# Optimization experiments

Measured on AMD Instinct MI355X. Metric: run time of the kernel, lower is better.

## Reference

```python
import jax, jax.numpy as jnp
import numpy as np

N_NODES = 50000
N_EDGES = 800000
IN_CH = 128
HEADS = 4
OUT_CH = 32
NEG_SLOPE = 0.2


def setup_inputs() -> dict:
    key = jax.random.key(0)
    ks = jax.random.split(key, 7)
    x = jax.random.normal(ks[0], (N_NODES, IN_CH), dtype=jnp.float32)
    src = jax.random.randint(ks[1], (N_EDGES,), 0, N_NODES, dtype=jnp.int32)
    dst = jax.random.randint(ks[2], (N_EDGES,), 0, N_NODES, dtype=jnp.int32)
    W = jax.random.normal(ks[3], (IN_CH, HEADS * OUT_CH), dtype=jnp.float32) * (1.0 / np.sqrt(IN_CH))
    attn_l = jax.random.normal(ks[4], (HEADS, OUT_CH), dtype=jnp.float32) * 0.1
    attn_r = jax.random.normal(ks[5], (HEADS, OUT_CH), dtype=jnp.float32) * 0.1
    bias = jnp.zeros((HEADS * OUT_CH,), dtype=jnp.float32)
    return {"x": x, "src": src, "dst": dst, "W": W, "attn_l": attn_l, "attn_r": attn_r, "bias": bias}


def reference(x, src, dst, W, attn_l, attn_r, bias):
    n = x.shape[0]
    # Linear projection -> per-head features [N, H, D]
    feat = (x @ W).reshape(n, HEADS, OUT_CH)
    # Node-level attention terms [N, H]
    el = jnp.einsum('nhd,hd->nh', feat, attn_l)
    er = jnp.einsum('nhd,hd->nh', feat, attn_r)
    # Edge attention logits [E, H]
    e = jax.nn.leaky_relu(el[src] + er[dst], negative_slope=NEG_SLOPE)
    # Segment softmax over incoming edges of each dst node
    m = jax.ops.segment_max(e, dst, num_segments=n)          # [N, H]
    m = jnp.where(jnp.isfinite(m), m, 0.0)
    ex = jnp.exp(e - m[dst])                                  # [E, H]
    s = jax.ops.segment_sum(ex, dst, num_segments=n)          # [N, H]
    alpha = ex / s[dst]                                       # [E, H]
    # Weighted message aggregation: scatter-add to dst [N, H, D]
    msg = feat[src] * alpha[:, :, None]
    out = jax.ops.segment_sum(msg, dst, num_segments=n)
    out = out + bias.reshape(HEADS, OUT_CH)
    # agg='mean' over heads -> [N, D]
    return out.mean(axis=1)
```

## Files before the change

### kernel.cpp

```cpp
#include <hip/hip_runtime.h>

#define IN_CH 128
#define NEG_SLOPE 0.2f
#define MAXDEG 64

typedef short bf16x8 __attribute__((ext_vector_type(8)));
typedef float floatx4 __attribute__((ext_vector_type(4)));

static __device__ __forceinline__ unsigned short f2bf(float f) {
    union { float f; unsigned int u; } a; a.f = f;
    unsigned int u = a.u;
    u += 0x7fffu + ((u >> 16) & 1u);
    return (unsigned short)(u >> 16);
}

__global__ void k_prep(const float* __restrict__ W, unsigned short* __restrict__ Wtb,
                       int* __restrict__ cnt, int N) {
    int i = blockIdx.x * 256 + threadIdx.x;
    if (i < N) cnt[(size_t)i << 4] = 0;
    if (i < 128 * 128) {
        int n = i >> 7, k = i & 127;
        Wtb[i] = f2bf(W[(size_t)k * 128 + n]);
    }
}

__global__ __launch_bounds__(256) void k_fused(const float* __restrict__ x,
                                               const unsigned short* __restrict__ Wtb,
                                               const float* __restrict__ attn_l,
                                               const float* __restrict__ attn_r,
                                               unsigned short* __restrict__ featb,
                                               float* __restrict__ el,
                                               float* __restrict__ er, int N,
                                               const int* __restrict__ src,
                                               const int* __restrict__ dst,
                                               int* __restrict__ cnt,
                                               unsigned short* __restrict__ esrc_pad, int E,
                                               int GB, int RB) {
    __shared__ __align__(16) unsigned short Al[16 * 136];
    __shared__ float elpart[2][8][16];
    int b = blockIdx.x;
    int M2 = 2 * (GB < RB ? GB : RB);
    bool is_edge;
    int part;
    if (b < M2) { is_edge = (b & 1); part = b >> 1; }
    else        { is_edge = (RB > GB); part = (M2 >> 1) + (b - M2); }
    if (is_edge) {
        int e = part * 256 + threadIdx.x;
        if (e < E) {
            int dn = dst[e];
            int sv = src[e];
            int r = atomicAdd(&cnt[(size_t)dn << 4], 1);
            if (r < MAXDEG) esrc_pad[(size_t)dn * MAXDEG + r] = (unsigned short)sv;
        }
        return;
    }
    int m0 = part * 16;
    const float4* xt = (const float4*)(x + (size_t)m0 * 128);
#pragma unroll
    for (int i = 0; i < 2; ++i) {
        int f4i = threadIdx.x + 256 * i;
        float4 u = xt[f4i];
        int f = f4i * 4;
        int row = f >> 7, col = f & 127;
        ushort4 pk;
        pk.x = f2bf(u.x); pk.y = f2bf(u.y); pk.z = f2bf(u.z); pk.w = f2bf(u.w);
        *(ushort4*)(Al + row * 136 + col) = pk;
    }
    __syncthreads();
    int wave = threadIdx.x >> 6;
    int lane = threadIdx.x & 63;
    int l15 = lane & 15;
    int quad = lane >> 4;
    int n0 = wave * 16;
    int n1 = wave * 16 + 64;
    const unsigned short* ap = Al + l15 * 136 + quad * 8;
    const unsigned short* bp0 = Wtb + (size_t)(n0 + l15) * 128 + quad * 8;
    const unsigned short* bp1 = Wtb + (size_t)(n1 + l15) * 128 + quad * 8;
    floatx4 acc0 = {0.f, 0.f, 0.f, 0.f};
    floatx4 acc1 = {0.f, 0.f, 0.f, 0.f};
#pragma unroll
    for (int kk = 0; kk < 4; ++kk) {
        bf16x8 a  = *(const bf16x8*)(ap + kk * 32);
        bf16x8 b0 = *(const bf16x8*)(bp0 + kk * 32);
        bf16x8 b1 = *(const bf16x8*)(bp1 + kk * 32);
        acc0 = __builtin_amdgcn_mfma_f32_16x16x32_bf16(a, b0, acc0, 0, 0, 0);
        acc1 = __builtin_amdgcn_mfma_f32_16x16x32_bf16(a, b1, acc1, 0, 0, 0);
    }
    float al0 = attn_l[n0 + l15], al1 = attn_l[n1 + l15];
    float ar0 = attn_r[n0 + l15], ar1 = attn_r[n1 + l15];
    float pl0[4], pl1[4], pr0[4], pr1[4];
#pragma unroll
    for (int r = 0; r < 4; ++r) {
        pl0[r] = acc0[r] * al0; pl1[r] = acc1[r] * al1;
        pr0[r] = acc0[r] * ar0; pr1[r] = acc1[r] * ar1;
#pragma unroll
        for (int m = 1; m <= 8; m <<= 1) {
            pl0[r] += __shfl_xor(pl0[r], m);
            pl1[r] += __shfl_xor(pl1[r], m);
            pr0[r] += __shfl_xor(pr0[r], m);
            pr1[r] += __shfl_xor(pr1[r], m);
        }
    }
    if (l15 == 0) {
#pragma unroll
        for (int r = 0; r < 4; ++r) {
            int row = quad * 4 + r;
            elpart[0][wave][row]     = pl0[r];
            elpart[0][wave + 4][row] = pl1[r];
            elpart[1][wave][row]     = pr0[r];
            elpart[1][wave + 4][row] = pr1[r];
        }
    }
#pragma unroll
    for (int r = 0; r < 4; ++r) {
        size_t row = (size_t)(m0 + quad * 4 + r) * 128;
        featb[row + n0 + l15] = f2bf(acc0[r]);
        featb[row + n1 + l15] = f2bf(acc1[r]);
    }
    __syncthreads();
    if (threadIdx.x < 128) {
        int lr = threadIdx.x >> 6;
        int t = threadIdx.x & 63;
        int row = t & 15, h = t >> 4;
        float v = elpart[lr][2 * h][row] + elpart[lr][2 * h + 1][row];
        float* dp = lr ? er : el;
        dp[(size_t)(m0 + row) * 4 + h] = v;
    }
}

__global__ __launch_bounds__(256) void k_node(const int* __restrict__ cnt,
                                              const unsigned short* __restrict__ esrc_pad,
                                              const float* __restrict__ el,
                                              const float* __restrict__ er,
                                              const unsigned short* __restrict__ featb,
                                              const float* __restrict__ bias,
                                              float* __restrict__ out, int N) {
    int n = blockIdx.x * 4 + (threadIdx.x >> 6);
    if (n >= N) return;
    int lane = threadIdx.x & 63;
    int g = lane >> 4;
    int r = lane & 15;
    int h = r >> 2;
    int deg = cnt[(size_t)n << 4];
    if (deg > MAXDEG) deg = MAXDEG;
    const unsigned short* ep = esrc_pad + (size_t)n * MAXDEG;
    float erh = er[(size_t)n * 4 + h];
    float s = 0.f;
    float a0 = 0.f, a1 = 0.f, a2 = 0.f, a3 = 0.f;
    float a4 = 0.f, a5 = 0.f, a6 = 0.f, a7 = 0.f;
    int j = g;
    int sn_c = (j < deg) ? (int)ep[j] : 0;
    float el_c = el[(size_t)sn_c * 4 + h];
    uint4 q_c = *(const uint4*)(featb + (size_t)sn_c * 128 + r * 8);
#pragma unroll 2
    for (; j < deg; j += 4) {
        int jn = j + 4;
        int sn_n = (jn < deg) ? (int)ep[jn] : 0;
        float el_n = el[(size_t)sn_n * 4 + h];
        uint4 q_n = *(const uint4*)(featb + (size_t)sn_n * 128 + r * 8);
        float t = el_c + erh;
        float e = __expf(t > 0.f ? t : NEG_SLOPE * t);
        s += e;
        a0 += e * __uint_as_float(q_c.x << 16);
        a1 += e * __uint_as_float(q_c.x & 0xffff0000u);
        a2 += e * __uint_as_float(q_c.y << 16);
        a3 += e * __uint_as_float(q_c.y & 0xffff0000u);
        a4 += e * __uint_as_float(q_c.z << 16);
        a5 += e * __uint_as_float(q_c.z & 0xffff0000u);
        a6 += e * __uint_as_float(q_c.w << 16);
        a7 += e * __uint_as_float(q_c.w & 0xffff0000u);
        sn_c = sn_n; el_c = el_n; q_c = q_n;
    }
    s  += __shfl_xor(s, 16);  s  += __shfl_xor(s, 32);
    a0 += __shfl_xor(a0, 16); a0 += __shfl_xor(a0, 32);
    a1 += __shfl_xor(a1, 16); a1 += __shfl_xor(a1, 32);
    a2 += __shfl_xor(a2, 16); a2 += __shfl_xor(a2, 32);
    a3 += __shfl_xor(a3, 16); a3 += __shfl_xor(a3, 32);
    a4 += __shfl_xor(a4, 16); a4 += __shfl_xor(a4, 32);
    a5 += __shfl_xor(a5, 16); a5 += __shfl_xor(a5, 32);
    a6 += __shfl_xor(a6, 16); a6 += __shfl_xor(a6, 32);
    a7 += __shfl_xor(a7, 16); a7 += __shfl_xor(a7, 32);
    float inv = (deg > 0) ? 0.25f / s : 0.f;
    a0 *= inv; a1 *= inv; a2 *= inv; a3 *= inv;
    a4 *= inv; a5 *= inv; a6 *= inv; a7 *= inv;
    a0 += __shfl_xor(a0, 4); a0 += __shfl_xor(a0, 8);
    a1 += __shfl_xor(a1, 4); a1 += __shfl_xor(a1, 8);
    a2 += __shfl_xor(a2, 4); a2 += __shfl_xor(a2, 8);
    a3 += __shfl_xor(a3, 4); a3 += __shfl_xor(a3, 8);
    a4 += __shfl_xor(a4, 4); a4 += __shfl_xor(a4, 8);
    a5 += __shfl_xor(a5, 4); a5 += __shfl_xor(a5, 8);
    a6 += __shfl_xor(a6, 4); a6 += __shfl_xor(a6, 8);
    a7 += __shfl_xor(a7, 4); a7 += __shfl_xor(a7, 8);
    if (lane < 4) {
        int dd = lane * 8;
        float4 o0, o1;
        o0.x = a0 + 0.25f * (bias[dd + 0] + bias[32 + dd + 0] + bias[64 + dd + 0] + bias[96 + dd + 0]);
        o0.y = a1 + 0.25f * (bias[dd + 1] + bias[32 + dd + 1] + bias[64 + dd + 1] + bias[96 + dd + 1]);
        o0.z = a2 + 0.25f * (bias[dd + 2] + bias[32 + dd + 2] + bias[64 + dd + 2] + bias[96 + dd + 2]);
        o0.w = a3 + 0.25f * (bias[dd + 3] + bias[32 + dd + 3] + bias[64 + dd + 3] + bias[96 + dd + 3]);
        o1.x = a4 + 0.25f * (bias[dd + 4] + bias[32 + dd + 4] + bias[64 + dd + 4] + bias[96 + dd + 4]);
        o1.y = a5 + 0.25f * (bias[dd + 5] + bias[32 + dd + 5] + bias[64 + dd + 5] + bias[96 + dd + 5]);
        o1.z = a6 + 0.25f * (bias[dd + 6] + bias[32 + dd + 6] + bias[64 + dd + 6] + bias[96 + dd + 6]);
        o1.w = a7 + 0.25f * (bias[dd + 7] + bias[32 + dd + 7] + bias[64 + dd + 7] + bias[96 + dd + 7]);
        *(float4*)(out + (size_t)n * 32 + dd) = o0;
        *(float4*)(out + (size_t)n * 32 + dd + 4) = o1;
    }
}

extern "C" void kernel_launch(void* const* d_in, const int* in_sizes, int n_in,
                              void* d_out, int out_size, void* d_ws, size_t ws_size,
                              hipStream_t stream) {
    const float* x      = (const float*)d_in[0];
    const int*   src    = (const int*)d_in[1];
    const int*   dst    = (const int*)d_in[2];
    const float* W      = (const float*)d_in[3];
    const float* attn_l = (const float*)d_in[4];
    const float* attn_r = (const float*)d_in[5];
    const float* bias   = (const float*)d_in[6];
    float* out = (float*)d_out;

    int N = in_sizes[0] / IN_CH;
    int E = in_sizes[1];
    int GB = N / 16;
    int RB = (E + 255) / 256;

    char* w = (char*)d_ws;
    unsigned short* featb = (unsigned short*)w; w += (size_t)N * 128 * 2;
    unsigned short* Wtb   = (unsigned short*)w; w += 128 * 128 * 2;
    float* el       = (float*)w;  w += (size_t)N * 4 * 4;
    float* er       = (float*)w;  w += (size_t)N * 4 * 4;
    int*   cnt      = (int*)w;    w += (size_t)N * 16 * 4;
    unsigned short* esrc_pad = (unsigned short*)w; w += (size_t)N * MAXDEG * 2;

    k_prep<<<(N + 255) / 256, 256, 0, stream>>>(W, Wtb, cnt, N);
    k_fused<<<GB + RB, 256, 0, stream>>>(x, Wtb, attn_l, attn_r, featb, el, er, N,
                                         src, dst, cnt, esrc_pad, E, GB, RB);
    k_node<<<(N + 3) / 4, 256, 0, stream>>>(cnt, esrc_pad, el, er, featb, bias, out, N);
}
```

Measured before the change: 154.5 us.

## Fold attention vectors into extra weight rows and tile GEMM blocks over 64 nodes

Precomputes W·attn_l and W·attn_r as eight extra bf16 rows of the weight matrix, so el/er come from a third MFMA instead of shuffle reductions and a shared-memory pass. Each GEMM block now stages the swizzled weight matrix in LDS and loops over four 16-row tiles, prefetching the next x tile into registers. Edge blocks handle four edges per thread using vector loads. The changes aim to cut global weight reads, block count and reduction overhead, at the cost of more LDS per block (lower occupancy), bf16 rounding of the folded attention weights, and an edge path that assumes E is a multiple of four.

```diff
diff --git a/kernel.cpp b/kernel.cpp
--- a/kernel.cpp
+++ b/kernel.cpp
@@ -3,6 +3,9 @@
 #define IN_CH 128
 #define NEG_SLOPE 0.2f
 #define MAXDEG 64
+
+#define GTILE 64
+#define EPB 1024
 
 typedef short bf16x8 __attribute__((ext_vector_type(8)));
 typedef float floatx4 __attribute__((ext_vector_type(4)));
@@ -14,20 +17,36 @@
     return (unsigned short)(u >> 16);
 }
 
-__global__ void k_prep(const float* __restrict__ W, unsigned short* __restrict__ Wtb,
+__global__ void k_prep(const float* __restrict__ W,
+                       const float* __restrict__ attn_l,
+                       const float* __restrict__ attn_r,
+                       unsigned short* __restrict__ Wtb2,
                        int* __restrict__ cnt, int N) {
     int i = blockIdx.x * 256 + threadIdx.x;
     if (i < N) cnt[(size_t)i << 4] = 0;
     if (i < 128 * 128) {
         int n = i >> 7, k = i & 127;
-        Wtb[i] = f2bf(W[(size_t)k * 128 + n]);
+        Wtb2[(size_t)n * 128 + k] = f2bf(W[(size_t)k * 128 + n]);
+    }
+    if (i < 1024) {
+        int row = i >> 7;
+        int k = i & 127;
+        int h = row & 3;
+        const float* av = (row < 4) ? attn_l : attn_r;
+        const float* wp = W + (size_t)k * 128 + h * 32;
+        float s = 0.f;
+#pragma unroll
+        for (int d = 0; d < 32; ++d) s += wp[d] * av[h * 32 + d];
+        Wtb2[(size_t)(128 + row) * 128 + k] = f2bf(s);
+    }
+    if (i >= 1024 && i < 2048) {
+        int row = 136 + ((i - 1024) >> 7);
+        Wtb2[(size_t)row * 128 + (i & 127)] = 0;
     }
 }
 
 __global__ __launch_bounds__(256) void k_fused(const float* __restrict__ x,
-                                               const unsigned short* __restrict__ Wtb,
-                                               const float* __restrict__ attn_l,
-                                               const float* __restrict__ attn_r,
+                                               const unsigned short* __restrict__ Wtb2,
                                                unsigned short* __restrict__ featb,
                                                float* __restrict__ el,
                                                float* __restrict__ er, int N,
@@ -36,95 +55,127 @@
                                                int* __restrict__ cnt,
                                                unsigned short* __restrict__ esrc_pad, int E,
                                                int GB, int RB) {
+    __shared__ __align__(16) unsigned short Bl[144 * 128];
     __shared__ __align__(16) unsigned short Al[16 * 136];
-    __shared__ float elpart[2][8][16];
     int b = blockIdx.x;
     int M2 = 2 * (GB < RB ? GB : RB);
     bool is_edge;
     int part;
     if (b < M2) { is_edge = (b & 1); part = b >> 1; }
     else        { is_edge = (RB > GB); part = (M2 >> 1) + (b - M2); }
+
     if (is_edge) {
-        int e = part * 256 + threadIdx.x;
-        if (e < E) {
-            int dn = dst[e];
-            int sv = src[e];
-            int r = atomicAdd(&cnt[(size_t)dn << 4], 1);
-            if (r < MAXDEG) esrc_pad[(size_t)dn * MAXDEG + r] = (unsigned short)sv;
+        int e0 = part * EPB + threadIdx.x * 4;
+        if (e0 < E) {
+            int4 s4 = *(const int4*)(src + e0);
+            int4 d4 = *(const int4*)(dst + e0);
+            int r0 = atomicAdd(&cnt[(size_t)d4.x << 4], 1);
+            int r1 = atomicAdd(&cnt[(size_t)d4.y << 4], 1);
+            int r2 = atomicAdd(&cnt[(size_t)d4.z << 4], 1);
+            int r3 = atomicAdd(&cnt[(size_t)d4.w << 4], 1);
+            if (r0 < MAXDEG) esrc_pad[(size_t)d4.x * MAXDEG + r0] = (unsigned short)s4.x;
+            if (r1 < MAXDEG) esrc_pad[(size_t)d4.y * MAXDEG + r1] = (unsigned short)s4.y;
+            if (r2 < MAXDEG) esrc_pad[(size_t)d4.z * MAXDEG + r2] = (unsigned short)s4.z;
+            if (r3 < MAXDEG) esrc_pad[(size_t)d4.w * MAXDEG + r3] = (unsigned short)s4.w;
         }
         return;
     }
-    int m0 = part * 16;
-    const float4* xt = (const float4*)(x + (size_t)m0 * 128);
-#pragma unroll
-    for (int i = 0; i < 2; ++i) {
-        int f4i = threadIdx.x + 256 * i;
-        float4 u = xt[f4i];
-        int f = f4i * 4;
-        int row = f >> 7, col = f & 127;
-        ushort4 pk;
-        pk.x = f2bf(u.x); pk.y = f2bf(u.y); pk.z = f2bf(u.z); pk.w = f2bf(u.w);
-        *(ushort4*)(Al + row * 136 + col) = pk;
-    }
-    __syncthreads();
+
+    int base = part * GTILE;
+    int ntile = (N - base + 15) >> 4; if (ntile > 4) ntile = 4;
+
+    {
+        const uint4* wsrc = (const uint4*)Wtb2;
+        char* blb = (char*)Bl;
+        for (int idx16 = threadIdx.x; idx16 < 2304; idx16 += 256) {
+            uint4 v = wsrc[idx16];
+            int n = idx16 >> 4;
+            int kb = (idx16 & 15) << 4;
+            *(uint4*)(blb + n * 256 + (kb ^ ((n & 7) << 4))) = v;
+        }
+    }
+
     int wave = threadIdx.x >> 6;
     int lane = threadIdx.x & 63;
     int l15 = lane & 15;
     int quad = lane >> 4;
-    int n0 = wave * 16;
-    int n1 = wave * 16 + 64;
-    const unsigned short* ap = Al + l15 * 136 + quad * 8;
-    const unsigned short* bp0 = Wtb + (size_t)(n0 + l15) * 128 + quad * 8;
-    const unsigned short* bp1 = Wtb + (size_t)(n1 + l15) * 128 + quad * 8;
-    floatx4 acc0 = {0.f, 0.f, 0.f, 0.f};
-    floatx4 acc1 = {0.f, 0.f, 0.f, 0.f};
-#pragma unroll
-    for (int kk = 0; kk < 4; ++kk) {
-        bf16x8 a  = *(const bf16x8*)(ap + kk * 32);
-        bf16x8 b0 = *(const bf16x8*)(bp0 + kk * 32);
-        bf16x8 b1 = *(const bf16x8*)(bp1 + kk * 32);
-        acc0 = __builtin_amdgcn_mfma_f32_16x16x32_bf16(a, b0, acc0, 0, 0, 0);
-        acc1 = __builtin_amdgcn_mfma_f32_16x16x32_bf16(a, b1, acc1, 0, 0, 0);
-    }
-    float al0 = attn_l[n0 + l15], al1 = attn_l[n1 + l15];
-    float ar0 = attn_r[n0 + l15], ar1 = attn_r[n1 + l15];
-    float pl0[4], pl1[4], pr0[4], pr1[4];
-#pragma unroll
-    for (int r = 0; r < 4; ++r) {
-        pl0[r] = acc0[r] * al0; pl1[r] = acc1[r] * al1;
-        pr0[r] = acc0[r] * ar0; pr1[r] = acc1[r] * ar1;
-#pragma unroll
-        for (int m = 1; m <= 8; m <<= 1) {
-            pl0[r] += __shfl_xor(pl0[r], m);
-            pl1[r] += __shfl_xor(pl1[r], m);
-            pr0[r] += __shfl_xor(pr0[r], m);
-            pr1[r] += __shfl_xor(pr1[r], m);
-        }
-    }
-    if (l15 == 0) {
+    int r0 = wave * 16 + l15;
+    int r1 = 64 + wave * 16 + l15;
+    int r2 = 128 + l15;
+    const char* blb = (const char*)Bl;
+    int sw = (l15 & 7) << 4;
+
+    float4 xr[2];
+    {
+        const float4* xt = (const float4*)(x + (size_t)base * 128);
+#pragma unroll
+        for (int i = 0; i < 2; ++i) {
+            float4 u = xt[threadIdx.x + 256 * i];
+            int f = (threadIdx.x + 256 * i) * 4;
+            int row = f >> 7, col = f & 127;
+            ushort4 pk;
+            pk.x = f2bf(u.x); pk.y = f2bf(u.y); pk.z = f2bf(u.z); pk.w = f2bf(u.w);
+            *(ushort4*)(Al + row * 136 + col) = pk;
+        }
+        if (ntile > 1) {
+            const float4* xt1 = (const float4*)(x + (size_t)(base + 16) * 128);
+#pragma unroll
+            for (int i = 0; i < 2; ++i) xr[i] = xt1[threadIdx.x + 256 * i];
+        }
+    }
+    __syncthreads();
+
+    for (int t = 0; t < ntile; ++t) {
+        int m0 = base + t * 16;
+        const unsigned short* ap = Al + l15 * 136 + quad * 8;
+        floatx4 acc0 = {0.f, 0.f, 0.f, 0.f};
+        floatx4 acc1 = {0.f, 0.f, 0.f, 0.f};
+        floatx4 acc2 = {0.f, 0.f, 0.f, 0.f};
+#pragma unroll
+        for (int kk = 0; kk < 4; ++kk) {
+            int kb = (quad << 4) + (kk << 6);
+            bf16x8 a  = *(const bf16x8*)(ap + kk * 32);
+            bf16x8 b0 = *(const bf16x8*)(blb + r0 * 256 + (kb ^ sw));
+            bf16x8 b1 = *(const bf16x8*)(blb + r1 * 256 + (kb ^ sw));
+            acc0 = __builtin_amdgcn_mfma_f32_16x16x32_bf16(a, b0, acc0, 0, 0, 0);
+            acc1 = __builtin_amdgcn_mfma_f32_16x16x32_bf16(a, b1, acc1, 0, 0, 0);
+            if (wave == 0) {
+                bf16x8 b2 = *(const bf16x8*)(blb + r2 * 256 + (kb ^ sw));
+                acc2 = __builtin_amdgcn_mfma_f32_16x16x32_bf16(a, b2, acc2, 0, 0, 0);
+            }
+        }
 #pragma unroll
         for (int r = 0; r < 4; ++r) {
-            int row = quad * 4 + r;
-            elpart[0][wave][row]     = pl0[r];
-            elpart[0][wave + 4][row] = pl1[r];
-            elpart[1][wave][row]     = pr0[r];
-            elpart[1][wave + 4][row] = pr1[r];
-        }
-    }
-#pragma unroll
-    for (int r = 0; r < 4; ++r) {
-        size_t row = (size_t)(m0 + quad * 4 + r) * 128;
-        featb[row + n0 + l15] = f2bf(acc0[r]);
-        featb[row + n1 + l15] = f2bf(acc1[r]);
-    }
-    __syncthreads();
-    if (threadIdx.x < 128) {
-        int lr = threadIdx.x >> 6;
-        int t = threadIdx.x & 63;
-        int row = t & 15, h = t >> 4;
-        float v = elpart[lr][2 * h][row] + elpart[lr][2 * h + 1][row];
-        float* dp = lr ? er : el;
-        dp[(size_t)(m0 + row) * 4 + h] = v;
+            size_t row = (size_t)(m0 + quad * 4 + r) * 128;
+            featb[row + r0] = f2bf(acc0[r]);
+            featb[row + r1] = f2bf(acc1[r]);
+        }
+        if (wave == 0) {
+#pragma unroll
+            for (int r = 0; r < 4; ++r) {
+                int m = m0 + quad * 4 + r;
+                if (l15 < 4)      el[(size_t)m * 4 + l15]       = acc2[r];
+                else if (l15 < 8) er[(size_t)m * 4 + (l15 - 4)] = acc2[r];
+            }
+        }
+        __syncthreads();
+        if (t + 1 < ntile) {
+#pragma unroll
+            for (int i = 0; i < 2; ++i) {
+                int f = (threadIdx.x + 256 * i) * 4;
+                int row = f >> 7, col = f & 127;
+                ushort4 pk;
+                pk.x = f2bf(xr[i].x); pk.y = f2bf(xr[i].y);
+                pk.z = f2bf(xr[i].z); pk.w = f2bf(xr[i].w);
+                *(ushort4*)(Al + row * 136 + col) = pk;
+            }
+            if (t + 2 < ntile) {
+                const float4* xt2 = (const float4*)(x + (size_t)(base + (t + 2) * 16) * 128);
+#pragma unroll
+                for (int i = 0; i < 2; ++i) xr[i] = xt2[threadIdx.x + 256 * i];
+            }
+        }
+        __syncthreads();
     }
 }
 
@@ -221,19 +272,19 @@
 
     int N = in_sizes[0] / IN_CH;
     int E = in_sizes[1];
-    int GB = N / 16;
-    int RB = (E + 255) / 256;
+    int GB = (N + GTILE - 1) / GTILE;
+    int RB = (E + EPB - 1) / EPB;
 
     char* w = (char*)d_ws;
     unsigned short* featb = (unsigned short*)w; w += (size_t)N * 128 * 2;
-    unsigned short* Wtb   = (unsigned short*)w; w += 128 * 128 * 2;
+    unsigned short* Wtb2  = (unsigned short*)w; w += 144 * 128 * 2;
     float* el       = (float*)w;  w += (size_t)N * 4 * 4;
     float* er       = (float*)w;  w += (size_t)N * 4 * 4;
     int*   cnt      = (int*)w;    w += (size_t)N * 16 * 4;
     unsigned short* esrc_pad = (unsigned short*)w; w += (size_t)N * MAXDEG * 2;
 
-    k_prep<<<(N + 255) / 256, 256, 0, stream>>>(W, Wtb, cnt, N);
-    k_fused<<<GB + RB, 256, 0, stream>>>(x, Wtb, attn_l, attn_r, featb, el, er, N,
+    k_prep<<<(N + 255) / 256, 256, 0, stream>>>(W, attn_l, attn_r, Wtb2, cnt, N);
+    k_fused<<<GB + RB, 256, 0, stream>>>(x, Wtb2, featb, el, er, N,
                                          src, dst, cnt, esrc_pad, E, GB, RB);
     k_node<<<(N + 3) / 4, 256, 0, stream>>>(cnt, esrc_pad, el, er, featb, bias, out, N);
 }
```

Result: no change. 154.7 us (+0.1%).
